# Kernel optimization log

Hardware: AMD Instinct MI355X
Metric: run time of the kernel (lower is better)

## Reference

```python
import jax, jax.numpy as jnp
import numpy as np

N_QUBITS = 12
N_LAYERS = 2
B, T, IN, H = 256, 32, 8, 128
TWO_PI = 2.0 * np.pi


def _apply_1q(state, U, w):
    # state: (B, 2,2,...,2) with N_QUBITS qubit axes; U: (2,2) or (B,2,2)
    s = jnp.moveaxis(state, w + 1, 1)
    if U.ndim == 3:
        s = jnp.einsum('bst,bt...->bs...', U, s)
    else:
        s = jnp.einsum('st,bt...->bs...', U, s)
    return jnp.moveaxis(s, 1, w + 1)


def _rx_batched(angles):
    # angles: (B,) -> (B,2,2) RX matrices
    c = jnp.cos(angles / 2).astype(jnp.complex64)
    s = jnp.sin(angles / 2).astype(jnp.complex64)
    row0 = jnp.stack([c, -1j * s], axis=-1)
    row1 = jnp.stack([-1j * s, c], axis=-1)
    return jnp.stack([row0, row1], axis=1)


def _rot(phi, theta, omega):
    # PennyLane Rot = RZ(omega) RY(theta) RZ(phi)
    c = jnp.cos(theta / 2).astype(jnp.complex64)
    s = jnp.sin(theta / 2).astype(jnp.complex64)
    ep = jnp.exp(-0.5j * (phi + omega).astype(jnp.complex64))
    em = jnp.exp(-0.5j * (phi - omega).astype(jnp.complex64))
    m00 = ep * c
    m01 = -jnp.conj(em) * s
    m10 = em * s
    m11 = jnp.conj(ep) * c
    return jnp.stack([jnp.stack([m00, m01]), jnp.stack([m10, m11])])


def _cnot(state, cw, tw):
    flipped = jnp.flip(state, axis=tw + 1)
    mask = jnp.arange(2).reshape([2 if a == cw + 1 else 1 for a in range(N_QUBITS + 1)])
    return jnp.where(mask == 1, flipped, state)


def _run_circuit(angles, qw):
    # angles: (B, N_QUBITS) embedding angles; qw: (L, N, 3)
    b = angles.shape[0]
    state = jnp.zeros((b, 2 ** N_QUBITS), jnp.complex64).at[:, 0].set(1.0)
    state = state.reshape((b,) + (2,) * N_QUBITS)
    for w in range(N_QUBITS):  # AngleEmbedding, rotation='X'
        state = _apply_1q(state, _rx_batched(angles[:, w]), w)
    for l in range(N_LAYERS):  # StronglyEntanglingLayers
        for w in range(N_QUBITS):
            state = _apply_1q(state, _rot(qw[l, w, 0], qw[l, w, 1], qw[l, w, 2]), w)
        r = (l % (N_QUBITS - 1)) + 1
        for w in range(N_QUBITS):
            state = _cnot(state, w, (w + r) % N_QUBITS)
    probs = state.real ** 2 + state.imag ** 2
    evs = []
    for i in range(4):  # <Z_i>
        sign = (1.0 - 2.0 * jnp.arange(2, dtype=probs.dtype)).reshape(
            [2 if a == i + 1 else 1 for a in range(N_QUBITS + 1)])
        evs.append(jnp.sum(probs * sign, axis=tuple(range(1, N_QUBITS + 1))))
    return jnp.stack(evs, axis=1)  # (B, 4)


def setup_inputs() -> dict:
    key = jax.random.key(0)
    ks = jax.random.split(key, 12)
    inp = {
        'x': jax.random.normal(ks[0], (B, T, IN), jnp.float32),
        'h0': jnp.zeros((B, H), jnp.float32),
        'c0': jnp.zeros((B, H), jnp.float32),
        'q_weights': jax.random.uniform(ks[1], (N_LAYERS, N_QUBITS, 3), jnp.float32) * TWO_PI,
        'Wf': jax.random.normal(ks[2], (H, 1), jnp.float32),
        'bf': jax.random.normal(ks[3], (H,), jnp.float32) * 0.1,
        'Wi': jax.random.normal(ks[4], (H, 1), jnp.float32),
        'bi': jax.random.normal(ks[5], (H,), jnp.float32) * 0.1,
        'Wc': jax.random.normal(ks[6], (H, 1), jnp.float32),
        'bc': jax.random.normal(ks[7], (H,), jnp.float32) * 0.1,
        'Wo': jax.random.normal(ks[8], (H, 1), jnp.float32),
        'bo': jax.random.normal(ks[9], (H,), jnp.float32) * 0.1,
    }
    return inp


def reference(x, h0, c0, q_weights, Wf, bf, Wi, bi, Wc, bc, Wo, bo):
    def step(carry, x_t):
        h, c = carry
        comb = jnp.concatenate([x_t, h], axis=1)[:, :N_QUBITS]  # truncate, matches source
        q = _run_circuit(comb, q_weights)  # (B, 4) expvals in [-1, 1]
        f = jax.nn.sigmoid(q[:, 0:1] @ Wf.T + bf)
        i = jax.nn.sigmoid(q[:, 1:2] @ Wi.T + bi)
        ct = jnp.tanh(q[:, 2:3] @ Wc.T + bc)
        o = jax.nn.sigmoid(q[:, 3:4] @ Wo.T + bo)
        c_new = f * c + i * ct
        h_new = o * jnp.tanh(c_new)
        return (h_new, c_new), None

    (h_t, c_t), _ = jax.lax.scan(step, (h0, c0), jnp.swapaxes(x, 0, 1))
    return h_t, c_t
```

## Files before the change

kernel.cpp:

```cpp
#include <hip/hip_runtime.h>
#include <math.h>

#define NQ 12
#define NS 4096
#define TT 32
#define BB 256
#define HH 128
#define NT 512

typedef float v2f __attribute__((ext_vector_type(2)));
typedef float v4f __attribute__((ext_vector_type(4)));

constexpr unsigned cnot_g(unsigned x, int w, int r){
    int pc = 11 - w;
    int pt = 11 - ((w + r) % 12);
    return x ^ (((x >> pc) & 1u) << pt);
}
constexpr unsigned Fperm(unsigned i, int r){
    unsigned x = i;
    for (int w = 11; w >= 0; --w) x = cnot_g(x, w, r);
    return x;
}
constexpr unsigned Finv(unsigned i, int r){
    unsigned x = i;
    for (int w = 0; w < 12; ++w) x = cnot_g(x, w, r);
    return x;
}
constexpr unsigned F0closed(unsigned i){
    return i ^ ((i >> 1) & 0x7FFu) ^ ((i & 1u) << 10) ^ ((i & 1u) << 11);
}
constexpr bool check_all(){
    for (int b = 0; b < NQ; ++b){
        const unsigned e = 1u << b;
        if (F0closed(e) != Fperm(e,1)) return false;
        if (Fperm(Finv(e,1),1) != e) return false;
        if (Fperm(Finv(e,2),2) != e) return false;
    }
    if (F0closed(0u) != 0u || Fperm(0u,1) != 0u || Finv(0u,2) != 0u) return false;
    if (F0closed(0x5A3u) != Fperm(0x5A3u,1)) return false;
    if (Fperm(Finv(0xABCu,2),2) != 0xABCu) return false;
    return true;
}
static_assert(check_all(), "CNOT permutation closed forms wrong");
constexpr unsigned maskM(int k){
    unsigned m = 0;
    for (int b = 0; b < NQ; ++b) m |= ((Finv(1u<<b, 2) >> (11 - k)) & 1u) << b;
    return m;
}
constexpr unsigned gM0 = maskM(0), gM1 = maskM(1), gM2 = maskM(2), gM3 = maskM(3);
constexpr int sgn9(unsigned M, int K){ return __builtin_popcount((unsigned)K & (M >> 9)) & 1; }

__device__ __forceinline__ v2f pk_cmul(v2f m, v2f a){
    v2f t;
    asm("v_pk_mul_f32 %0, %1, %2 op_sel:[0,0] op_sel_hi:[0,1]"
        : "=v"(t) : "v"(m), "v"(a));
    asm("v_pk_fma_f32 %0, %1, %2, %0 op_sel:[1,1,0] op_sel_hi:[1,0,1] neg_lo:[1,0,0]"
        : "+v"(t) : "v"(m), "v"(a));
    return t;
}
__device__ __forceinline__ v2f pk_cfma(v2f m, v2f a, v2f acc){
    asm("v_pk_fma_f32 %0, %1, %2, %0 op_sel:[0,0,0] op_sel_hi:[0,1,1]"
        : "+v"(acc) : "v"(m), "v"(a));
    asm("v_pk_fma_f32 %0, %1, %2, %0 op_sel:[1,1,0] op_sel_hi:[1,0,1] neg_lo:[1,0,0]"
        : "+v"(acc) : "v"(m), "v"(a));
    return acc;
}
template<int NL, int NH>
__device__ __forceinline__ void pk_accsgn(v2f &acc, v2f ppb){
    if constexpr (NL==0 && NH==0)
        asm("v_pk_add_f32 %0, %1, %0" : "+v"(acc) : "v"(ppb));
    else if constexpr (NL==1 && NH==0)
        asm("v_pk_add_f32 %0, %1, %0 neg_lo:[1,0]" : "+v"(acc) : "v"(ppb));
    else if constexpr (NL==0 && NH==1)
        asm("v_pk_add_f32 %0, %1, %0 neg_hi:[1,0]" : "+v"(acc) : "v"(ppb));
    else
        asm("v_pk_add_f32 %0, %1, %0 neg_lo:[1,0] neg_hi:[1,0]" : "+v"(acc) : "v"(ppb));
}
template<int K>
__device__ __forceinline__ void expk(const v2f* amp, v2f &a01, v2f &a23){
    const float pp = fmaf(amp[K].x, amp[K].x, amp[K].y * amp[K].y);
    v2f ppb; ppb.x = pp; ppb.y = pp;
    pk_accsgn<sgn9(gM0,K), sgn9(gM1,K)>(a01, ppb);
    pk_accsgn<sgn9(gM2,K), sgn9(gM3,K)>(a23, ppb);
    if constexpr (K < 7) expk<K+1>(amp, a01, a23);
}

template<int C>
__device__ __forceinline__ float dppadd(float v){
    return v + __int_as_float(
        __builtin_amdgcn_update_dpp(0, __float_as_int(v), C, 0xF, 0xF, true));
}
__device__ __forceinline__ float wsum(float v){
    v = dppadd<0x111>(v);
    v = dppadd<0x112>(v);
    v = dppadd<0x114>(v);
    v = dppadd<0x118>(v);
    v = dppadd<0x142>(v);
    v = dppadd<0x143>(v);
    return v;
}


__device__ __forceinline__ float fsig(float xv){ return __fdividef(1.f, 1.f + __expf(-xv)); }
__device__ __forceinline__ float ftanh(float xv){
    const float e = __expf(-2.f * xv);
    return __fdividef(1.f - e, 1.f + e);
}

template<int WTOP>
__device__ __forceinline__ void rot3r(v2f* s, const v2f (&G)[NQ][4]){
    #pragma unroll
    for (int lb = 0; lb < 3; ++lb){
        const v2f M00 = G[WTOP-lb][0], M01 = G[WTOP-lb][1];
        const v2f M10 = G[WTOP-lb][2], M11 = G[WTOP-lb][3];
        #pragma unroll
        for (int k = 0; k < 8; ++k){
            if (k & (1 << lb)) continue;
            const int k1 = k | (1 << lb);
            const v2f a = s[k], b = s[k1];
            s[k]  = pk_cfma(M01, b, pk_cmul(M00, a));
            s[k1] = pk_cfma(M11, b, pk_cmul(M10, a));
        }
    }
}

extern "C" __global__ void __launch_bounds__(NT)
qlstm_kernel(const float* __restrict__ x,  const float* __restrict__ h0,
             const float* __restrict__ c0, const float* __restrict__ qw,
             const float* __restrict__ Wf, const float* __restrict__ bfp,
             const float* __restrict__ Wi, const float* __restrict__ bip,
             const float* __restrict__ Wc, const float* __restrict__ bcp,
             const float* __restrict__ Wo, const float* __restrict__ bop,
             float* __restrict__ out)
{
    __shared__ v2f S[NS];
    __shared__ v2f matp[2][NQ][4];
    __shared__ v2f vvx[8][2];
    __shared__ v4f vvh[8][4];
    __shared__ float xs[TT*8];
    __shared__ float4 red4[8];

    const int b    = blockIdx.x;
    const int tid  = threadIdx.x;
    const int wave = tid >> 6;
    const int lane = tid & 63;

    if (tid < 2*NQ){
        const int l = tid / NQ, w = tid % NQ;
        const float phi = qw[(l*NQ + w)*3 + 0];
        const float th  = qw[(l*NQ + w)*3 + 1];
        const float om  = qw[(l*NQ + w)*3 + 2];
        float cth, sth, cap, sap, cam, sam;
        sincosf(0.5f*th, &sth, &cth);
        sincosf(0.5f*(phi+om), &sap, &cap);
        sincosf(0.5f*(phi-om), &sam, &cam);
        v2f m00; m00.x =  cap*cth; m00.y = -sap*cth;
        v2f m01; m01.x = -cam*sth; m01.y = -sam*sth;
        v2f m10; m10.x =  cam*sth; m10.y = -sam*sth;
        v2f m11; m11.x =  cap*cth; m11.y =  sap*cth;
        matp[l][w][0] = m00; matp[l][w][1] = m01;
        matp[l][w][2] = m10; matp[l][w][3] = m11;
    }
    if (tid >= 256) xs[tid - 256] = x[b*(TT*8) + (tid - 256)];

    float wf=0,bfv=0,wi=0,biv=0,wc=0,bcv=0,wo=0,bov=0,c_reg=0,h_reg=0;
    if (tid < HH){
        c_reg = c0[b*HH + tid];  h_reg = h0[b*HH + tid];
        wf=Wf[tid]; bfv=bfp[tid]; wi=Wi[tid]; biv=bip[tid];
        wc=Wc[tid]; bcv=bcp[tid]; wo=Wo[tid]; bov=bop[tid];
    }
    const int cw = tid & 3;
    const float WfC=Wf[cw], bfC=bfp[cw], WiC=Wi[cw], biC=bip[cw];
    const float WcC=Wc[cw], bcC=bcp[cw], WoC=Wo[cw], boC=bop[cw];
    float c4 = c0[b*HH + cw];
    const float h_init = h0[b*HH + cw];
    __syncthreads();

    const v2f M8w0 = matp[0][8+cw][0], M8w1 = matp[0][8+cw][1];
    const v2f M8w2 = matp[0][8+cw][2], M8w3 = matp[0][8+cw][3];

    v2f G[NQ][4];
    #pragma unroll
    for (int w = 0; w < NQ; ++w)
        #pragma unroll
        for (int m = 0; m < 4; ++m) G[w][m] = matp[1][w][m];

    if (tid >= 128 && tid < 136){
        const int w = tid - 128;
        float sa, ca; sincosf(0.5f*xs[w], &sa, &ca);
        const v2f M00=matp[0][w][0], M01=matp[0][w][1], M10=matp[0][w][2], M11=matp[0][w][3];
        v2f t0v; t0v.x = M00.x*ca + M01.y*sa; t0v.y = M00.y*ca - M01.x*sa;
        v2f t1v; t1v.x = M10.x*ca + M11.y*sa; t1v.y = M10.y*ca - M11.x*sa;
        vvx[w][0] = t0v; vvx[w][1] = t1v;
    }
    v4f hv0, hv1, hv2, hv3;
    {
        float sa, ca; sincosf(0.5f*h_init, &sa, &ca);
        v4f hw;
        hw.x = M8w0.x*ca + M8w1.y*sa;  hw.y = M8w0.y*ca - M8w1.x*sa;
        hw.z = M8w2.x*ca + M8w3.y*sa;  hw.w = M8w2.y*ca - M8w3.x*sa;
        if (lane < 4) vvh[wave][lane] = hw;
        asm volatile("" ::: "memory");
        hv0 = vvh[wave][0]; hv1 = vvh[wave][1]; hv2 = vvh[wave][2]; hv3 = vvh[wave][3];
    }
    __syncthreads();

    const float sg0 = (__builtin_parity(tid & (gM0 & 0x1FFu)) ? -1.f : 1.f);
    const float sg1 = (__builtin_parity(tid & (gM1 & 0x1FFu)) ? -1.f : 1.f);
    const float sg2 = (__builtin_parity(tid & (gM2 & 0x1FFu)) ? -1.f : 1.f);
    const float sg3 = (__builtin_parity(tid & (gM3 & 0x1FFu)) ? -1.f : 1.f);
    const int bA = (tid << 3) ^ (tid & 31);
    const int bB = (tid & 7) ^ (((tid >> 3) & 3) << 3) ^ ((tid >> 3) << 6);
    const int bC = ((tid & 63) ^ ((tid >> 3) & 7)) | ((tid >> 6) << 9);
    const int bD = tid ^ ((tid >> 3) & 31);
    const int s2 = ((tid>>6) ^ (tid>>7)) & 1;
    const int s3 = ((tid>>5) ^ (tid>>6)) & 1;
    const int s4 = ((tid>>4) ^ (tid>>5)) & 1;
    const int s5 = ((tid>>3) ^ (tid>>4)) & 1;
    const int s6 = ((tid>>2) ^ (tid>>3)) & 1;
    const int s7 = ((tid>>1) ^ (tid>>2)) & 1;
    const int s8 = ( tid     ^ (tid>>1)) & 1;
    const int t8  = (tid >> 8) & 1;
    const int t78 = ((tid>>7) ^ (tid>>8)) & 1;
    const int t0  = tid & 1;
    const v2f* vf = &vvx[0][0];

    v2f amp[8];

    #pragma unroll 1
    for (int t = 0; t < TT; ++t){
        const v2f e2 = vf[ 4+s2], e3 = vf[ 6+s3], e4 = vf[ 8+s4];
        const v2f e5 = vf[10+s5], e6 = vf[12+s6], e7 = vf[14+s7];
        v2f e8; e8.x = s8 ? hv0.z : hv0.x;  e8.y = s8 ? hv0.w : hv0.y;
        const v2f Q  = pk_cmul(pk_cmul(pk_cmul(e2,e3), pk_cmul(e4,e5)),
                               pk_cmul(pk_cmul(e6,e7), e8));
        const v2f v0a = vf[0], v0b = vf[1], v1a = vf[2], v1b = vf[3];
        const v2f ua0 = t8 ? v0b : v0a,  ua1 = t8 ? v0a : v0b;
        const v2f ub0 = t78 ? v1b : v1a, ub1 = t78 ? v1a : v1b;
        const v2f QU0 = pk_cmul(Q, pk_cmul(ua0, ub0));
        const v2f QU1 = pk_cmul(Q, pk_cmul(ua1, ub1));
        v2f v9a; v9a.x = hv1.x; v9a.y = hv1.y;
        v2f v9b; v9b.x = hv1.z; v9b.y = hv1.w;
        const v2f v9s0 = t0 ? v9b : v9a, v9s1 = t0 ? v9a : v9b;
        v2f v10a; v10a.x = hv2.x; v10a.y = hv2.y;
        v2f v10b; v10b.x = hv2.z; v10b.y = hv2.w;
        v2f v11a; v11a.x = hv3.x; v11a.y = hv3.y;
        v2f v11b; v11b.x = hv3.z; v11b.y = hv3.w;
        const v2f P2_0 = pk_cmul(v10a, v11a), P2_1 = pk_cmul(v10a, v11b);
        const v2f P2_2 = pk_cmul(v10b, v11a), P2_3 = pk_cmul(v10b, v11b);
        #pragma unroll
        for (int k = 0; k < 8; ++k){
            const int g = k ^ (k >> 1);
            const v2f base = (k & 1) ? QU1 : QU0;
            const v2f w9   = (g & 4) ? v9s1 : v9s0;
            const v2f p2   = (g&3)==0 ? P2_0 : (g&3)==1 ? P2_1 : (g&3)==2 ? P2_2 : P2_3;
            amp[k] = pk_cmul(pk_cmul(base, w9), p2);
        }

        rot3r<11>(amp, G);
        #pragma unroll
        for (int k = 0; k < 8; ++k) S[bA ^ k] = amp[k];
        asm volatile("" ::: "memory");
        #pragma unroll
        for (int k = 0; k < 8; ++k) amp[k] = S[bB ^ (9*k)];
        rot3r<8>(amp, G);
        #pragma unroll
        for (int k = 0; k < 8; ++k) S[bB ^ (9*k)] = amp[k];
        asm volatile("" ::: "memory");
        #pragma unroll
        for (int k = 0; k < 8; ++k) amp[k] = S[bC ^ ((k<<6) | ((k&3)<<3))];
        rot3r<5>(amp, G);
        #pragma unroll
        for (int k = 0; k < 8; ++k) S[bC ^ ((k<<6) | ((k&3)<<3))] = amp[k];
        __syncthreads();
        #pragma unroll
        for (int k = 0; k < 8; ++k) amp[k] = S[bD + (k<<9)];
        rot3r<2>(amp, G);

        v2f a01; a01.x = 0.f; a01.y = 0.f;
        v2f a23; a23.x = 0.f; a23.y = 0.f;
        expk<0>(amp, a01, a23);
        float p0 = a01.x * sg0, p1 = a01.y * sg1;
        float p2s = a23.x * sg2, p3 = a23.y * sg3;
        p0 = wsum(p0); p1 = wsum(p1); p2s = wsum(p2s); p3 = wsum(p3);
        if (lane == 63) red4[wave] = make_float4(p0, p1, p2s, p3);
        if (tid >= 128 && tid < 136){
            const int w  = tid - 128;
            const int tn = (t + 1 < TT) ? t + 1 : t;
            float sa, ca; __sincosf(0.5f*xs[tn*8 + w], &sa, &ca);
            const v2f M00=matp[0][w][0], M01=matp[0][w][1], M10=matp[0][w][2], M11=matp[0][w][3];
            v2f t0v; t0v.x = M00.x*ca + M01.y*sa; t0v.y = M00.y*ca - M01.x*sa;
            v2f t1v; t1v.x = M10.x*ca + M11.y*sa; t1v.y = M10.y*ca - M11.x*sa;
            vvx[w][0] = t0v; vvx[w][1] = t1v;
        }
        __syncthreads();

        float q0=0.f, q1=0.f, q2=0.f, q3=0.f;
        #pragma unroll
        for (int i = 0; i < 8; ++i){
            const float4 r = red4[i];
            q0 += r.x; q1 += r.y; q2 += r.z; q3 += r.w;
        }
        {
            const float fg = fsig (q0*WfC + bfC);
            const float ig = fsig (q1*WiC + biC);
            const float cg = ftanh(q2*WcC + bcC);
            const float og = fsig (q3*WoC + boC);
            c4 = fg*c4 + ig*cg;
            const float hj = og * ftanh(c4);
            float sa, ca; __sincosf(0.5f*hj, &sa, &ca);
            v4f hw;
            hw.x = M8w0.x*ca + M8w1.y*sa;  hw.y = M8w0.y*ca - M8w1.x*sa;
            hw.z = M8w2.x*ca + M8w3.y*sa;  hw.w = M8w2.y*ca - M8w3.x*sa;
            if (lane < 4) vvh[wave][lane] = hw;
            asm volatile("" ::: "memory");
            hv0 = vvh[wave][0]; hv1 = vvh[wave][1];
            hv2 = vvh[wave][2]; hv3 = vvh[wave][3];
        }
        if (tid < HH){
            const float fg = fsig (q0*wf + bfv);
            const float ig = fsig (q1*wi + biv);
            const float cg = ftanh(q2*wc + bcv);
            const float og = fsig (q3*wo + bov);
            c_reg = fg*c_reg + ig*cg;
            h_reg = og * ftanh(c_reg);
        }
    }

    if (tid < HH){
        out[b*HH + tid]          = h_reg;
        out[BB*HH + b*HH + tid]  = c_reg;
    }
}

extern "C" void kernel_launch(void* const* d_in, const int* in_sizes, int n_in,
                              void* d_out, int out_size, void* d_ws, size_t ws_size,
                              hipStream_t stream)
{
    (void)in_sizes; (void)n_in; (void)d_ws; (void)ws_size; (void)out_size;
    const float* x  = (const float*)d_in[0];
    const float* h0 = (const float*)d_in[1];
    const float* c0 = (const float*)d_in[2];
    const float* qw = (const float*)d_in[3];
    const float* Wf = (const float*)d_in[4];
    const float* bf = (const float*)d_in[5];
    const float* Wi = (const float*)d_in[6];
    const float* bi = (const float*)d_in[7];
    const float* Wc = (const float*)d_in[8];
    const float* bc = (const float*)d_in[9];
    const float* Wo = (const float*)d_in[10];
    const float* bo = (const float*)d_in[11];
    qlstm_kernel<<<BB, NT, 0, stream>>>(x, h0, c0, qw, Wf, bf, Wi, bi,
                                        Wc, bc, Wo, bo, (float*)d_out);
}
```

Measured before the change: 108.3 us.

## Factor layer-2 Rot into diagonal phases plus real RY rotations; defer full-H LSTM

The second layer's Rot gates are split algebraically. The RZ(phi) phases are folded into per-thread diagonal factors (Zphi, dd[k]) that multiply the state before the CNOT/rotation stage, so each butterfly becomes a real-coefficient RY rotation instead of a full complex 2x2 multiply. The per-step 128-wide LSTM update is removed from the time loop: the step's q values go into shared memory and the full hidden state is replayed once after the loop. This cuts ALU work in the inner rotation stages and the serial per-step critical path, but it relies on the phase commuting correctly through the remaining RY gates and the CNOT permutation.

```diff
diff --git a/kernel.cpp b/kernel.cpp
--- a/kernel.cpp
+++ b/kernel.cpp
@@ -57,13 +57,6 @@
     asm("v_pk_fma_f32 %0, %1, %2, %0 op_sel:[1,1,0] op_sel_hi:[1,0,1] neg_lo:[1,0,0]"
         : "+v"(t) : "v"(m), "v"(a));
     return t;
-}
-__device__ __forceinline__ v2f pk_cfma(v2f m, v2f a, v2f acc){
-    asm("v_pk_fma_f32 %0, %1, %2, %0 op_sel:[0,0,0] op_sel_hi:[0,1,1]"
-        : "+v"(acc) : "v"(m), "v"(a));
-    asm("v_pk_fma_f32 %0, %1, %2, %0 op_sel:[1,1,0] op_sel_hi:[1,0,1] neg_lo:[1,0,0]"
-        : "+v"(acc) : "v"(m), "v"(a));
-    return acc;
 }
 template<int NL, int NH>
 __device__ __forceinline__ void pk_accsgn(v2f &acc, v2f ppb){
@@ -108,18 +101,17 @@
 }
 
 template<int WTOP>
-__device__ __forceinline__ void rot3r(v2f* s, const v2f (&G)[NQ][4]){
+__device__ __forceinline__ void rot3ry(v2f* s, const v2f* G){
     #pragma unroll
     for (int lb = 0; lb < 3; ++lb){
-        const v2f M00 = G[WTOP-lb][0], M01 = G[WTOP-lb][1];
-        const v2f M10 = G[WTOP-lb][2], M11 = G[WTOP-lb][3];
+        const float cw = G[WTOP-lb].x, sw = G[WTOP-lb].y;
         #pragma unroll
         for (int k = 0; k < 8; ++k){
             if (k & (1 << lb)) continue;
             const int k1 = k | (1 << lb);
             const v2f a = s[k], b = s[k1];
-            s[k]  = pk_cfma(M01, b, pk_cmul(M00, a));
-            s[k1] = pk_cfma(M11, b, pk_cmul(M10, a));
+            s[k]  = a*cw - b*sw;
+            s[k1] = a*sw + b*cw;
         }
     }
 }
@@ -134,22 +126,23 @@
              float* __restrict__ out)
 {
     __shared__ v2f S[NS];
-    __shared__ v2f matp[2][NQ][4];
+    __shared__ v2f matp[NQ][4];
     __shared__ v2f vvx[8][2];
     __shared__ v4f vvh[8][4];
     __shared__ float xs[TT*8];
     __shared__ float4 red4[8];
+    __shared__ float4 qh[TT];
 
     const int b    = blockIdx.x;
     const int tid  = threadIdx.x;
     const int wave = tid >> 6;
     const int lane = tid & 63;
 
-    if (tid < 2*NQ){
-        const int l = tid / NQ, w = tid % NQ;
-        const float phi = qw[(l*NQ + w)*3 + 0];
-        const float th  = qw[(l*NQ + w)*3 + 1];
-        const float om  = qw[(l*NQ + w)*3 + 2];
+    if (tid < NQ){
+        const int w = tid;
+        const float phi = qw[w*3 + 0];
+        const float th  = qw[w*3 + 1];
+        const float om  = qw[w*3 + 2];
         float cth, sth, cap, sap, cam, sam;
         sincosf(0.5f*th, &sth, &cth);
         sincosf(0.5f*(phi+om), &sap, &cap);
@@ -158,17 +151,41 @@
         v2f m01; m01.x = -cam*sth; m01.y = -sam*sth;
         v2f m10; m10.x =  cam*sth; m10.y = -sam*sth;
         v2f m11; m11.x =  cap*cth; m11.y =  sap*cth;
-        matp[l][w][0] = m00; matp[l][w][1] = m01;
-        matp[l][w][2] = m10; matp[l][w][3] = m11;
+        matp[w][0] = m00; matp[w][1] = m01;
+        matp[w][2] = m10; matp[w][3] = m11;
     }
     if (tid >= 256) xs[tid - 256] = x[b*(TT*8) + (tid - 256)];
 
-    float wf=0,bfv=0,wi=0,biv=0,wc=0,bcv=0,wo=0,bov=0,c_reg=0,h_reg=0;
-    if (tid < HH){
-        c_reg = c0[b*HH + tid];  h_reg = h0[b*HH + tid];
-        wf=Wf[tid]; bfv=bfp[tid]; wi=Wi[tid]; biv=bip[tid];
-        wc=Wc[tid]; bcv=bcp[tid]; wo=Wo[tid]; bov=bop[tid];
-    }
+    v2f G[NQ];
+    #pragma unroll
+    for (int w = 0; w < NQ; ++w){
+        float cg, sg; sincosf(0.5f*qw[(NQ + w)*3 + 1], &sg, &cg);
+        G[w].x = cg; G[w].y = sg;
+    }
+    v2f Zphi;
+    {
+        float A = 0.f;
+        #pragma unroll
+        for (int w = 0; w <= 8; ++w){
+            const float ph = qw[(NQ + w)*3 + 0];
+            A += ((tid >> (8 - w)) & 1) ? ph : -ph;
+        }
+        float sa, ca; sincosf(0.5f*A, &sa, &ca);
+        Zphi.x = ca; Zphi.y = sa;
+    }
+    v2f dd[8];
+    {
+        const float p9  = qw[(NQ + 9)*3 + 0];
+        const float p10 = qw[(NQ +10)*3 + 0];
+        const float p11 = qw[(NQ +11)*3 + 0];
+        #pragma unroll
+        for (int k = 0; k < 8; ++k){
+            const float Bq = 0.5f*(((k&4)? p9 : -p9) + ((k&2)? p10 : -p10) + ((k&1)? p11 : -p11));
+            float sb, cb; sincosf(Bq, &sb, &cb);
+            dd[k].x = cb; dd[k].y = sb;
+        }
+    }
+
     const int cw = tid & 3;
     const float WfC=Wf[cw], bfC=bfp[cw], WiC=Wi[cw], biC=bip[cw];
     const float WcC=Wc[cw], bcC=bcp[cw], WoC=Wo[cw], boC=bop[cw];
@@ -176,19 +193,13 @@
     const float h_init = h0[b*HH + cw];
     __syncthreads();
 
-    const v2f M8w0 = matp[0][8+cw][0], M8w1 = matp[0][8+cw][1];
-    const v2f M8w2 = matp[0][8+cw][2], M8w3 = matp[0][8+cw][3];
-
-    v2f G[NQ][4];
-    #pragma unroll
-    for (int w = 0; w < NQ; ++w)
-        #pragma unroll
-        for (int m = 0; m < 4; ++m) G[w][m] = matp[1][w][m];
+    const v2f M8w0 = matp[8+cw][0], M8w1 = matp[8+cw][1];
+    const v2f M8w2 = matp[8+cw][2], M8w3 = matp[8+cw][3];
 
     if (tid >= 128 && tid < 136){
         const int w = tid - 128;
         float sa, ca; sincosf(0.5f*xs[w], &sa, &ca);
-        const v2f M00=matp[0][w][0], M01=matp[0][w][1], M10=matp[0][w][2], M11=matp[0][w][3];
+        const v2f M00=matp[w][0], M01=matp[w][1], M10=matp[w][2], M11=matp[w][3];
         v2f t0v; t0v.x = M00.x*ca + M01.y*sa; t0v.y = M00.y*ca - M01.x*sa;
         v2f t1v; t1v.x = M10.x*ca + M11.y*sa; t1v.y = M10.y*ca - M11.x*sa;
         vvx[w][0] = t0v; vvx[w][1] = t1v;
@@ -233,7 +244,7 @@
         const v2f e5 = vf[10+s5], e6 = vf[12+s6], e7 = vf[14+s7];
         v2f e8; e8.x = s8 ? hv0.z : hv0.x;  e8.y = s8 ? hv0.w : hv0.y;
         const v2f Q  = pk_cmul(pk_cmul(pk_cmul(e2,e3), pk_cmul(e4,e5)),
-                               pk_cmul(pk_cmul(e6,e7), e8));
+                               pk_cmul(pk_cmul(e6,e7), pk_cmul(e8, Zphi)));
         const v2f v0a = vf[0], v0b = vf[1], v1a = vf[2], v1b = vf[3];
         const v2f ua0 = t8 ? v0b : v0a,  ua1 = t8 ? v0a : v0b;
         const v2f ub0 = t78 ? v1b : v1a, ub1 = t78 ? v1a : v1b;
@@ -254,28 +265,28 @@
             const v2f base = (k & 1) ? QU1 : QU0;
             const v2f w9   = (g & 4) ? v9s1 : v9s0;
             const v2f p2   = (g&3)==0 ? P2_0 : (g&3)==1 ? P2_1 : (g&3)==2 ? P2_2 : P2_3;
-            amp[k] = pk_cmul(pk_cmul(base, w9), p2);
-        }
-
-        rot3r<11>(amp, G);
+            amp[k] = pk_cmul(pk_cmul(base, w9), pk_cmul(p2, dd[k]));
+        }
+
+        rot3ry<11>(amp, G);
         #pragma unroll
         for (int k = 0; k < 8; ++k) S[bA ^ k] = amp[k];
         asm volatile("" ::: "memory");
         #pragma unroll
         for (int k = 0; k < 8; ++k) amp[k] = S[bB ^ (9*k)];
-        rot3r<8>(amp, G);
+        rot3ry<8>(amp, G);
         #pragma unroll
         for (int k = 0; k < 8; ++k) S[bB ^ (9*k)] = amp[k];
         asm volatile("" ::: "memory");
         #pragma unroll
         for (int k = 0; k < 8; ++k) amp[k] = S[bC ^ ((k<<6) | ((k&3)<<3))];
-        rot3r<5>(amp, G);
+        rot3ry<5>(amp, G);
         #pragma unroll
         for (int k = 0; k < 8; ++k) S[bC ^ ((k<<6) | ((k&3)<<3))] = amp[k];
         __syncthreads();
         #pragma unroll
         for (int k = 0; k < 8; ++k) amp[k] = S[bD + (k<<9)];
-        rot3r<2>(amp, G);
+        rot3ry<2>(amp, G);
 
         v2f a01; a01.x = 0.f; a01.y = 0.f;
         v2f a23; a23.x = 0.f; a23.y = 0.f;
@@ -288,7 +299,7 @@
             const int w  = tid - 128;
             const int tn = (t + 1 < TT) ? t + 1 : t;
             float sa, ca; __sincosf(0.5f*xs[tn*8 + w], &sa, &ca);
-            const v2f M00=matp[0][w][0], M01=matp[0][w][1], M10=matp[0][w][2], M11=matp[0][w][3];
+            const v2f M00=matp[w][0], M01=matp[w][1], M10=matp[w][2], M11=matp[w][3];
             v2f t0v; t0v.x = M00.x*ca + M01.y*sa; t0v.y = M00.y*ca - M01.x*sa;
             v2f t1v; t1v.x = M10.x*ca + M11.y*sa; t1v.y = M10.y*ca - M11.x*sa;
             vvx[w][0] = t0v; vvx[w][1] = t1v;
@@ -301,6 +312,7 @@
             const float4 r = red4[i];
             q0 += r.x; q1 += r.y; q2 += r.z; q3 += r.w;
         }
+        if (tid == 0) qh[t] = make_float4(q0, q1, q2, q3);
         {
             const float fg = fsig (q0*WfC + bfC);
             const float ig = fsig (q1*WiC + biC);
@@ -317,19 +329,26 @@
             hv0 = vvh[wave][0]; hv1 = vvh[wave][1];
             hv2 = vvh[wave][2]; hv3 = vvh[wave][3];
         }
-        if (tid < HH){
-            const float fg = fsig (q0*wf + bfv);
-            const float ig = fsig (q1*wi + biv);
-            const float cg = ftanh(q2*wc + bcv);
-            const float og = fsig (q3*wo + bov);
-            c_reg = fg*c_reg + ig*cg;
-            h_reg = og * ftanh(c_reg);
-        }
-    }
-
+    }
+
+    __syncthreads();
     if (tid < HH){
-        out[b*HH + tid]          = h_reg;
-        out[BB*HH + b*HH + tid]  = c_reg;
+        const float wfE=Wf[tid], bfE=bfp[tid], wiE=Wi[tid], biE=bip[tid];
+        const float wcE=Wc[tid], bcE=bcp[tid], woE=Wo[tid], boE=bop[tid];
+        float cc = c0[b*HH + tid];
+        float hh = 0.f;
+        #pragma unroll 1
+        for (int t = 0; t < TT; ++t){
+            const float4 q = qh[t];
+            const float fg = fsig (q.x*wfE + bfE);
+            const float ig = fsig (q.y*wiE + biE);
+            const float cg = ftanh(q.z*wcE + bcE);
+            const float og = fsig (q.w*woE + boE);
+            cc = fg*cc + ig*cg;
+            hh = og * ftanh(cc);
+        }
+        out[b*HH + tid]         = hh;
+        out[BB*HH + b*HH + tid] = cc;
     }
 }
 
```

Measured after the change: 104.1 us. 3.9% less time.
